# Kernel tuning notes

Hardware: AMD Instinct MI355X
Metric: run time of the kernel (lower is better)

Reference implementation:

```python
import jax, jax.numpy as jnp
import numpy as np

N_NODES = 50000
N_EDGES = 1600000
F_IN = 128
HIDDEN = 128
NUM_GRAPHS = 64


def _glorot(key, shape):
    fan_in = shape[0]
    return (jax.random.normal(key, shape, dtype=jnp.float32) / np.sqrt(fan_in)).astype(jnp.float32)


def setup_inputs() -> dict:
    key = jax.random.key(0)
    ks = jax.random.split(key, 16)
    x = jax.random.normal(ks[0], (N_NODES, F_IN), dtype=jnp.float32)
    edge_index = jax.random.randint(ks[1], (2, N_EDGES), 0, N_NODES, dtype=jnp.int64)
    batch = jnp.sort(jax.random.randint(ks[2], (N_NODES,), 0, NUM_GRAPHS, dtype=jnp.int64))
    # SAGEConv params: lin_l acts on aggregated neighbors, lin_r on root features.
    params = {
        'Wl0': _glorot(ks[3], (F_IN, HIDDEN)), 'Wr0': _glorot(ks[4], (F_IN, HIDDEN)), 'b0': jnp.zeros((HIDDEN,), jnp.float32),
        'Wl1': _glorot(ks[5], (HIDDEN, HIDDEN)), 'Wr1': _glorot(ks[6], (HIDDEN, HIDDEN)), 'b1': jnp.zeros((HIDDEN,), jnp.float32),
        'Wl2': _glorot(ks[7], (HIDDEN, HIDDEN)), 'Wr2': _glorot(ks[8], (HIDDEN, HIDDEN)), 'b2': jnp.zeros((HIDDEN,), jnp.float32),
        'W_lin1': _glorot(ks[9], (3 * HIDDEN, HIDDEN)), 'b_lin1': jnp.zeros((HIDDEN,), jnp.float32),
        'W_lin2': _glorot(ks[10], (HIDDEN, 2)), 'b_lin2': jnp.zeros((2,), jnp.float32),
    }
    return {'x': x, 'edge_index': edge_index, 'batch': batch, **params}


def _sage_conv(x, src, dst, Wl, Wr, b):
    # mean-aggregate neighbor (source) features at target nodes
    n = x.shape[0]
    deg = jax.ops.segment_sum(jnp.ones(src.shape, x.dtype), dst, num_segments=n)
    agg = jax.ops.segment_sum(x[src], dst, num_segments=n)
    agg = agg / jnp.maximum(deg, 1.0)[:, None]
    return agg @ Wl + x @ Wr + b


def reference(x, edge_index, batch,
              Wl0, Wr0, b0, Wl1, Wr1, b1, Wl2, Wr2, b2,
              W_lin1, b_lin1, W_lin2, b_lin2):
    src, dst = edge_index[0], edge_index[1]
    h = jax.nn.relu(_sage_conv(x, src, dst, Wl0, Wr0, b0))
    h = jax.nn.relu(_sage_conv(h, src, dst, Wl1, Wr1, b1))
    h = jax.nn.relu(_sage_conv(h, src, dst, Wl2, Wr2, b2))
    # global add / mean / max pool over graph ids
    add_p = jax.ops.segment_sum(h, batch, num_segments=NUM_GRAPHS)
    cnt = jax.ops.segment_sum(jnp.ones((h.shape[0],), h.dtype), batch, num_segments=NUM_GRAPHS)
    mean_p = add_p / jnp.maximum(cnt, 1.0)[:, None]
    max_p = jax.ops.segment_max(h, batch, num_segments=NUM_GRAPHS)
    g = jnp.concatenate([add_p, mean_p, max_p], axis=1)  # [G, 3*hidden]
    g = jax.nn.relu(g @ W_lin1 + b_lin1)
    # dropout p=0.5 is identity in eval mode
    logits = g @ W_lin2 + b_lin2
    return jax.nn.log_softmax(logits, axis=-1)
```

## Files before the change

kernel.cpp:

```cpp
#include <hip/hip_runtime.h>
#include <hip/hip_bf16.h>

#define N_NODES   50000
#define ZROW      N_NODES
#define F         128
#define NGRAPH    64
#define NB        391
#define B1        400
#define PADMAX    384

typedef __attribute__((ext_vector_type(8))) short    bf16x8;
typedef __attribute__((ext_vector_type(4))) float    f32x4;
typedef __attribute__((ext_vector_type(4))) unsigned u32x4;

__global__ __launch_bounds__(256) void bucket_hist(const int* __restrict__ dst,
                                                   int* __restrict__ bh, int nE, int chunk) {
    __shared__ int hist[NB];
    for (int i = threadIdx.x; i < NB; i += 256) hist[i] = 0;
    __syncthreads();
    int e0 = blockIdx.x * chunk;
    int e1 = min(e0 + chunk, nE);
    for (int e = e0 + threadIdx.x; e < e1; e += 256)
        atomicAdd(&hist[dst[e] >> 7], 1);
    __syncthreads();
    for (int i = threadIdx.x; i < NB; i += 256)
        bh[i * B1 + blockIdx.x] = hist[i];
}

__global__ __launch_bounds__(512) void scan_blocks(const int* __restrict__ bh,
                                                   int* __restrict__ boff,
                                                   int* __restrict__ btot) {
    __shared__ int s[512];
    int bkt = blockIdx.x, t = threadIdx.x;
    int v = (t < B1) ? bh[bkt * B1 + t] : 0;
    s[t] = v;
    __syncthreads();
    for (int off = 1; off < 512; off <<= 1) {
        int u = (t >= off) ? s[t - off] : 0;
        __syncthreads();
        s[t] += u;
        __syncthreads();
    }
    if (t < B1) boff[bkt * B1 + t] = s[t] - v;
    if (t == B1 - 1) btot[bkt] = s[t];
}

__global__ __launch_bounds__(512) void scan_buckets(const int* __restrict__ btot,
                                                    int* __restrict__ bbase) {
    __shared__ int s[512];
    int t = threadIdx.x;
    int v = (t < NB) ? btot[t] : 0;
    s[t] = v;
    __syncthreads();
    for (int off = 1; off < 512; off <<= 1) {
        int u = (t >= off) ? s[t - off] : 0;
        __syncthreads();
        s[t] += u;
        __syncthreads();
    }
    if (t < NB) bbase[t] = s[t] - v;
    if (t == NB - 1) bbase[NB] = s[t];
}

__global__ __launch_bounds__(256) void bucket_place(const int* __restrict__ src,
                                                    const int* __restrict__ dst,
                                                    const int* __restrict__ boff,
                                                    const int* __restrict__ bbase,
                                                    ushort2* __restrict__ ebuf, int nE, int chunk) {
    __shared__ int cur[NB];
    for (int i = threadIdx.x; i < NB; i += 256)
        cur[i] = bbase[i] + boff[i * B1 + blockIdx.x];
    __syncthreads();
    int e0 = blockIdx.x * chunk;
    int e1 = min(e0 + chunk, nE);
    for (int e = e0 + threadIdx.x; e < e1; e += 256) {
        int d = dst[e];
        int pos = atomicAdd(&cur[d >> 7], 1);
        ebuf[pos] = make_ushort2((unsigned short)src[e], (unsigned short)(d & 127));
    }
}

__global__ __launch_bounds__(256) void csr_build(const ushort2* __restrict__ ebuf,
                                                 const int* __restrict__ bbase,
                                                 int* __restrict__ row_ptr,
                                                 int* __restrict__ deg_arr,
                                                 unsigned short* __restrict__ csr, int n) {
    __shared__ int hist[128];
    __shared__ int cursor[128];
    __shared__ int pend[128];
    int b = blockIdx.x, t = threadIdx.x;
    int e0 = bbase[b], e1 = bbase[b + 1];
    if (t < 128) hist[t] = 0;
    __syncthreads();
    for (int e = e0 + t; e < e1; e += 256)
        atomicAdd(&hist[ebuf[e].y], 1);
    __syncthreads();
    if (t == 0) {
        int run = e0 + b * PADMAX;
        #pragma unroll 4
        for (int i = 0; i < 128; ++i) { cursor[i] = run; run += (hist[i] + 3) & ~3; }
    }
    __syncthreads();
    int node = b * 128 + t;
    if (t < 128) {
        pend[t] = cursor[t] + ((hist[t] + 3) & ~3);
        if (node < n) { row_ptr[node] = cursor[t]; deg_arr[node] = hist[t]; }
    }
    __syncthreads();
    for (int e = e0 + t; e < e1; e += 256) {
        ushort2 ed = ebuf[e];
        int pos = atomicAdd(&cursor[ed.y], 1);
        csr[pos] = ed.x;
    }
    __syncthreads();
    if (t < 128)
        for (int p = cursor[t]; p < pend[t]; ++p) csr[p] = (unsigned short)ZROW;
}

struct bh4 { __hip_bfloat16 a, b, c, d; };
__global__ __launch_bounds__(256) void cvt_kernel(const float* __restrict__ in,
                                                  __hip_bfloat16* __restrict__ out, long n4) {
    long i = (long)blockIdx.x * 256 + threadIdx.x;
    if (i >= n4) return;
    float4 v = ((const float4*)in)[i];
    bh4 o;
    o.a = __float2bfloat16(v.x);
    o.b = __float2bfloat16(v.y);
    o.c = __float2bfloat16(v.z);
    o.d = __float2bfloat16(v.w);
    ((bh4*)out)[i] = o;
}

__global__ __launch_bounds__(64) void zero_rows(__hip_bfloat16* __restrict__ xb,
                                                __hip_bfloat16* __restrict__ h1,
                                                __hip_bfloat16* __restrict__ h2) {
    int t = threadIdx.x;
    if (t < 48) {
        __hip_bfloat16* base = (t < 16) ? xb : (t < 32) ? h1 : h2;
        ((u32x4*)(base + (long)ZROW * F))[t & 15] = (u32x4){0, 0, 0, 0};
    }
}

__device__ __forceinline__ void acc8(float* a, u32x4 v) {
    a[0] += __uint_as_float(v.x << 16); a[1] += __uint_as_float(v.x & 0xffff0000u);
    a[2] += __uint_as_float(v.y << 16); a[3] += __uint_as_float(v.y & 0xffff0000u);
    a[4] += __uint_as_float(v.z << 16); a[5] += __uint_as_float(v.z & 0xffff0000u);
    a[6] += __uint_as_float(v.w << 16); a[7] += __uint_as_float(v.w & 0xffff0000u);
}

__global__ __launch_bounds__(256) void gather_kernel(const __hip_bfloat16* __restrict__ xin,
                                                     const int* __restrict__ row_ptr,
                                                     const int* __restrict__ deg_arr,
                                                     const unsigned short* __restrict__ csr,
                                                     __hip_bfloat16* __restrict__ agg, int n) {
    const int node = blockIdx.x * 4 + (threadIdx.x >> 6);
    if (node >= n) return;
    const int lane = threadIdx.x & 63;
    const int q = lane >> 4;
    const int r = lane & 15;

    const int beg = __builtin_nontemporal_load(&row_ptr[node]);
    const int d   = __builtin_nontemporal_load(&deg_arr[node]);
    const int end = beg + ((d + 3) & ~3);

    const u32x4* __restrict__ xr4 = (const u32x4*)xin;

    float a[8] = {}, b[8] = {};
    int i = beg;
    for (; i + 15 < end; i += 16) {
        int s0 = (int)__builtin_nontemporal_load(&csr[i + q]);
        int s1 = (int)__builtin_nontemporal_load(&csr[i + 4 + q]);
        int s2 = (int)__builtin_nontemporal_load(&csr[i + 8 + q]);
        int s3 = (int)__builtin_nontemporal_load(&csr[i + 12 + q]);
        u32x4 v0 = xr4[(unsigned)s0 * 16u + r];
        u32x4 v1 = xr4[(unsigned)s1 * 16u + r];
        u32x4 v2 = xr4[(unsigned)s2 * 16u + r];
        u32x4 v3 = xr4[(unsigned)s3 * 16u + r];
        acc8(a, v0);
        acc8(b, v1);
        acc8(a, v2);
        acc8(b, v3);
    }
    for (; i < end; i += 4) {
        int s0 = (int)__builtin_nontemporal_load(&csr[i + q]);
        u32x4 v0 = xr4[(unsigned)s0 * 16u + r];
        acc8(a, v0);
    }
    #pragma unroll
    for (int j = 0; j < 8; ++j) a[j] += b[j];

    #pragma unroll
    for (int j = 0; j < 8; ++j) {
        a[j] += __shfl_xor(a[j], 16);
        a[j] += __shfl_xor(a[j], 32);
    }

    if (q == 0) {
        float inv = 1.f / fmaxf((float)d, 1.f);
        u32x4 res;
        #pragma unroll
        for (int k = 0; k < 4; ++k) {
            __hip_bfloat16 lo = __float2bfloat16(a[2 * k]     * inv);
            __hip_bfloat16 hi = __float2bfloat16(a[2 * k + 1] * inv);
            res[k] = (unsigned)*(unsigned short*)&lo | ((unsigned)*(unsigned short*)&hi << 16);
        }
        __builtin_nontemporal_store(res, &((u32x4*)agg)[(long)node * 16 + r]);
    }
}

__global__ __launch_bounds__(256) void wfrag_all(const float* __restrict__ Wl0, const float* __restrict__ Wr0,
                                                 const float* __restrict__ Wl1, const float* __restrict__ Wr1,
                                                 const float* __restrict__ Wl2, const float* __restrict__ Wr2,
                                                 __hip_bfloat16* __restrict__ Wf) {
    int layer = blockIdx.x >> 4;
    int t = (blockIdx.x & 15) * 256 + threadIdx.x;
    const float* Wl = (layer == 0) ? Wl0 : (layer == 1) ? Wl1 : Wl2;
    const float* Wr = (layer == 0) ? Wr0 : (layer == 1) ? Wr1 : Wr2;
    int frag = t >> 6, lane = t & 63;
    int kstep = frag >> 3, ntg = frag & 7;
    int q = lane >> 4, r = lane & 15;
    bf16x8 v;
    #pragma unroll
    for (int j = 0; j < 8; ++j) {
        int krow = kstep * 32 + q * 8 + j;
        int col  = ntg * 16 + r;
        float f  = (krow < 128) ? Wl[krow * F + col] : Wr[(krow - 128) * F + col];
        __hip_bfloat16 h = __float2bfloat16(f);
        v[j] = *(short*)&h;
    }
    ((bf16x8*)(Wf + (long)layer * 32768))[t] = v;
}

__global__ __launch_bounds__(256) void sage_gemm(const __hip_bfloat16* __restrict__ aggb,
                                                 const __hip_bfloat16* __restrict__ hinb,
                                                 const __hip_bfloat16* __restrict__ Wf,
                                                 const float* __restrict__ bias,
                                                 __hip_bfloat16* __restrict__ hout,
                                                 const int* __restrict__ batch,
                                                 float* __restrict__ add_p,
                                                 unsigned* __restrict__ max_p,
                                                 float* __restrict__ cnt,
                                                 int n, int do_pool) {
    __shared__ __align__(16) __hip_bfloat16 sOut[64 * 128];
    __shared__ int sBatch[64];

    const int tid  = threadIdx.x;
    const int base = blockIdx.x * 64;
    const int w    = tid >> 6;
    const int lane = tid & 63;
    const int wr   = w >> 1, wc = w & 1;
    const int q    = lane >> 4, r = lane & 15;
    const int m0   = base + wr * 32;

    if (do_pool && tid < 64 && base + tid < n) sBatch[tid] = batch[base + tid];

    int rowA0 = m0 + r;        if (rowA0 >= n) rowA0 = 0;
    int rowA1 = m0 + 16 + r;   if (rowA1 >= n) rowA1 = 0;
    const long a0 = (long)rowA0 * 128 + q * 8;
    const long a1 = (long)rowA1 * 128 + q * 8;

    f32x4 acc[2][4];
    #pragma unroll
    for (int s = 0; s < 2; ++s)
        #pragma unroll
        for (int t = 0; t < 4; ++t) acc[s][t] = (f32x4){0.f, 0.f, 0.f, 0.f};

    const bf16x8* __restrict__ Wv = (const bf16x8*)Wf;
    #pragma unroll
    for (int kstep = 0; kstep < 8; ++kstep) {
        const __hip_bfloat16* basep = (kstep < 4) ? aggb : hinb;
        const int ko = (kstep & 3) * 32;
        bf16x8 af0 = *(const bf16x8*)(basep + a0 + ko);
        bf16x8 af1 = *(const bf16x8*)(basep + a1 + ko);
        #pragma unroll
        for (int t = 0; t < 4; ++t) {
            bf16x8 bf = Wv[(kstep * 8 + wc * 4 + t) * 64 + lane];
            acc[0][t] = __builtin_amdgcn_mfma_f32_16x16x32_bf16(af0, bf, acc[0][t], 0, 0, 0);
            acc[1][t] = __builtin_amdgcn_mfma_f32_16x16x32_bf16(af1, bf, acc[1][t], 0, 0, 0);
        }
    }

    if (!do_pool) {
        #pragma unroll
        for (int t = 0; t < 4; ++t) {
            int col = wc * 64 + t * 16 + r;
            float bv = bias[col];
            #pragma unroll
            for (int s = 0; s < 2; ++s) {
                #pragma unroll
                for (int j = 0; j < 4; ++j) {
                    int rowD = m0 + s * 16 + q * 4 + j;
                    if (rowD < n) {
                        float v = fmaxf(acc[s][t][j] + bv, 0.f);
                        hout[(long)rowD * F + col] = __float2bfloat16(v);
                    }
                }
            }
        }
    } else {
        #pragma unroll
        for (int t = 0; t < 4; ++t) {
            int col = wc * 64 + t * 16 + r;
            float bv = bias[col];
            #pragma unroll
            for (int s = 0; s < 2; ++s) {
                #pragma unroll
                for (int j = 0; j < 4; ++j) {
                    int rowl = wr * 32 + s * 16 + q * 4 + j;
                    float v = fmaxf(acc[s][t][j] + bv, 0.f);
                    sOut[rowl * 128 + col] = __float2bfloat16(v);
                }
            }
        }
        __syncthreads();
        const int colv = tid & 127, rh = tid >> 7;
        float s = 0.f, mx = 0.f, ct = 0.f;
        int g = -1;
        for (int row = rh * 32; row < rh * 32 + 32; ++row) {
            int m = base + row;
            if (m >= n) break;
            int gm = sBatch[row];
            if (gm != g) {
                if (g >= 0) {
                    atomicAdd(&add_p[g * F + colv], s);
                    atomicMax(&max_p[g * F + colv], __float_as_uint(mx));
                    if (colv == 0) atomicAdd(&cnt[g], ct);
                }
                s = 0.f; mx = 0.f; ct = 0.f; g = gm;
            }
            float v = __bfloat162float(sOut[row * 128 + colv]);
            s += v;
            mx = fmaxf(mx, v);
            ct += 1.f;
        }
        if (g >= 0) {
            atomicAdd(&add_p[g * F + colv], s);
            atomicMax(&max_p[g * F + colv], __float_as_uint(mx));
            if (colv == 0) atomicAdd(&cnt[g], ct);
        }
    }
}

__global__ __launch_bounds__(128) void head_kernel(const float* __restrict__ add_p,
                                                   const float* __restrict__ cnt,
                                                   const unsigned* __restrict__ max_p,
                                                   const float* __restrict__ W1,
                                                   const float* __restrict__ b1,
                                                   const float* __restrict__ W2,
                                                   const float* __restrict__ b2,
                                                   float* __restrict__ out) {
    int g = blockIdx.x, n = threadIdx.x;
    __shared__ float gv[384];
    float a    = add_p[g * F + n];
    float invc = 1.f / fmaxf(cnt[g], 1.f);
    gv[n]       = a;
    gv[128 + n] = a * invc;
    gv[256 + n] = __uint_as_float(max_p[g * F + n]);
    __syncthreads();

    float acc = b1[n];
    #pragma unroll 8
    for (int k = 0; k < 384; ++k) acc += gv[k] * W1[k * F + n];
    float r = fmaxf(acc, 0.f);

    float l0 = r * W2[n * 2 + 0];
    float l1 = r * W2[n * 2 + 1];
    #pragma unroll
    for (int off = 32; off > 0; off >>= 1) {
        l0 += __shfl_down(l0, off);
        l1 += __shfl_down(l1, off);
    }
    __shared__ float part[4];
    if ((n & 63) == 0) { part[(n >> 6) * 2] = l0; part[(n >> 6) * 2 + 1] = l1; }
    __syncthreads();
    if (n == 0) {
        float L0 = part[0] + part[2] + b2[0];
        float L1 = part[1] + part[3] + b2[1];
        float m  = fmaxf(L0, L1);
        float lse = m + logf(expf(L0 - m) + expf(L1 - m));
        out[g * 2 + 0] = L0 - lse;
        out[g * 2 + 1] = L1 - lse;
    }
}

extern "C" void kernel_launch(void* const* d_in, const int* in_sizes, int n_in,
                              void* d_out, int out_size, void* d_ws, size_t ws_size,
                              hipStream_t stream) {
    const float* x     = (const float*)d_in[0];
    const int*   ei    = (const int*)d_in[1];
    const int*   batch = (const int*)d_in[2];
    const float* Wl0 = (const float*)d_in[3];
    const float* Wr0 = (const float*)d_in[4];
    const float* b0  = (const float*)d_in[5];
    const float* Wl1 = (const float*)d_in[6];
    const float* Wr1 = (const float*)d_in[7];
    const float* b1  = (const float*)d_in[8];
    const float* Wl2 = (const float*)d_in[9];
    const float* Wr2 = (const float*)d_in[10];
    const float* b2  = (const float*)d_in[11];
    const float* W_lin1 = (const float*)d_in[12];
    const float* b_lin1 = (const float*)d_in[13];
    const float* W_lin2 = (const float*)d_in[14];
    const float* b_lin2 = (const float*)d_in[15];

    const int nE = in_sizes[1] / 2;
    const int* src = ei;
    const int* dst = ei + nE;

    const long TROWS = N_NODES + 16;
    char* p = (char*)d_ws;
    int*   row_ptr = (int*)p;            p += 50048 * 4;
    int*   deg_arr = (int*)p;            p += 50048 * 4;
    unsigned short* csr = (unsigned short*)p;  p += (((long)nE + (long)NB * PADMAX + 63) & ~63L) * 2;
    int*   bh      = (int*)p;            p += ((long)NB * B1 + 16) * 4;
    int*   boff    = (int*)p;            p += ((long)NB * B1 + 16) * 4;
    int*   btot    = (int*)p;            p += 512 * 4;
    int*   bbase   = (int*)p;            p += 512 * 4;
    __hip_bfloat16* xb   = (__hip_bfloat16*)p; p += TROWS * F * 2;
    __hip_bfloat16* aggb = (__hip_bfloat16*)p; p += TROWS * F * 2;
    __hip_bfloat16* h1b  = (__hip_bfloat16*)p; p += TROWS * F * 2;
    __hip_bfloat16* h2b  = (__hip_bfloat16*)p; p += TROWS * F * 2;
    __hip_bfloat16* Wf   = (__hip_bfloat16*)p; p += 3L * 32768 * 2;
    float* add_p   = (float*)p;          p += NGRAPH * F * 4;
    unsigned* max_p = (unsigned*)p;      p += NGRAPH * F * 4;
    float* cnt     = (float*)p;          p += 256;

    ushort2* ebuf = (ushort2*)aggb;

    const int chunk = (nE + B1 - 1) / B1;
    const int gridG = (N_NODES + 63) / 64;
    const int gridW = (N_NODES + 3) / 4;
    const int gridC = (int)(((long)N_NODES * F / 4 + 255) / 256);

    bucket_hist <<<B1, 256, 0, stream>>>(dst, bh, nE, chunk);
    scan_blocks <<<NB, 512, 0, stream>>>(bh, boff, btot);
    scan_buckets<<<1,  512, 0, stream>>>(btot, bbase);
    bucket_place<<<B1, 256, 0, stream>>>(src, dst, boff, bbase, ebuf, nE, chunk);
    csr_build   <<<NB, 256, 0, stream>>>(ebuf, bbase, row_ptr, deg_arr, csr, N_NODES);

    cvt_kernel<<<gridC, 256, 0, stream>>>(x, xb, (long)N_NODES * F / 4);
    zero_rows<<<1, 64, 0, stream>>>(xb, h1b, h2b);
    wfrag_all<<<48, 256, 0, stream>>>(Wl0, Wr0, Wl1, Wr1, Wl2, Wr2, Wf);
    hipMemsetAsync(add_p, 0, (NGRAPH * F * 2 + NGRAPH) * sizeof(float), stream);

    gather_kernel<<<gridW, 256, 0, stream>>>(xb, row_ptr, deg_arr, csr, aggb, N_NODES);
    sage_gemm<<<gridG, 256, 0, stream>>>(aggb, xb, Wf, b0, h1b,
                                         batch, add_p, max_p, cnt, N_NODES, 0);
    gather_kernel<<<gridW, 256, 0, stream>>>(h1b, row_ptr, deg_arr, csr, aggb, N_NODES);
    sage_gemm<<<gridG, 256, 0, stream>>>(aggb, h1b, Wf + 32768, b1, h2b,
                                         batch, add_p, max_p, cnt, N_NODES, 0);
    gather_kernel<<<gridW, 256, 0, stream>>>(h2b, row_ptr, deg_arr, csr, aggb, N_NODES);
    sage_gemm<<<gridG, 256, 0, stream>>>(aggb, h2b, Wf + 65536, b2, (__hip_bfloat16*)nullptr,
                                         batch, add_p, max_p, cnt, N_NODES, 1);

    head_kernel<<<NGRAPH, 128, 0, stream>>>(add_p, cnt, max_p,
                                            W_lin1, b_lin1, W_lin2, b_lin2,
                                            (float*)d_out);
}
```

Measured before the change: 281.9 us.

## Fuse preprocessing kernels into one launch, shrink histogram blocks, pack row pointer and degree

Merges the bucket histogram, fp32-to-bf16 conversion of x, weight fragment packing, pool zeroing and zero-row setup into a single prep_kernel that dispatches on block index. This removes several launches and the memset, and lets these independent jobs run concurrently. The histogram/placement block count drops from 400 to 128, so the scan uses 128-thread blocks. row_ptr and degree are now interleaved into one int2 array so the gather reads both with a single 64-bit load. Fewer histogram blocks mean each one handles a longer chunk, which may slow the histogram and placement stages.

```diff
diff --git a/kernel.cpp b/kernel.cpp
--- a/kernel.cpp
+++ b/kernel.cpp
@@ -6,42 +6,103 @@
 #define F         128
 #define NGRAPH    64
 #define NB        391
-#define B1        400
+#define B1        128
+#define B1ALLOC   400
 #define PADMAX    384
+
+#define CVT_BLOCKS 6250
+#define P_HIST_END 128
+#define P_CVT_END  (P_HIST_END + CVT_BLOCKS)
+#define P_WF_END   (P_CVT_END + 48)
+#define P_ZERO_END (P_WF_END + 65)
+#define P_GRID     (P_ZERO_END + 1)
+#define POOL_FLOATS (NGRAPH * F * 2 + NGRAPH)
 
 typedef __attribute__((ext_vector_type(8))) short    bf16x8;
 typedef __attribute__((ext_vector_type(4))) float    f32x4;
 typedef __attribute__((ext_vector_type(4))) unsigned u32x4;
 
-__global__ __launch_bounds__(256) void bucket_hist(const int* __restrict__ dst,
-                                                   int* __restrict__ bh, int nE, int chunk) {
-    __shared__ int hist[NB];
-    for (int i = threadIdx.x; i < NB; i += 256) hist[i] = 0;
-    __syncthreads();
-    int e0 = blockIdx.x * chunk;
-    int e1 = min(e0 + chunk, nE);
-    for (int e = e0 + threadIdx.x; e < e1; e += 256)
-        atomicAdd(&hist[dst[e] >> 7], 1);
-    __syncthreads();
-    for (int i = threadIdx.x; i < NB; i += 256)
-        bh[i * B1 + blockIdx.x] = hist[i];
-}
-
-__global__ __launch_bounds__(512) void scan_blocks(const int* __restrict__ bh,
+struct bh4 { __hip_bfloat16 a, b, c, d; };
+
+__global__ __launch_bounds__(256) void prep_kernel(const int* __restrict__ dst, int nE, int chunk,
+                                                   int* __restrict__ bh,
+                                                   const float* __restrict__ x,
+                                                   __hip_bfloat16* __restrict__ xb,
+                                                   const float* __restrict__ Wl0, const float* __restrict__ Wr0,
+                                                   const float* __restrict__ Wl1, const float* __restrict__ Wr1,
+                                                   const float* __restrict__ Wl2, const float* __restrict__ Wr2,
+                                                   __hip_bfloat16* __restrict__ Wf,
+                                                   float* __restrict__ poolz,
+                                                   __hip_bfloat16* __restrict__ h1,
+                                                   __hip_bfloat16* __restrict__ h2) {
+    const int b   = blockIdx.x;
+    const int tid = threadIdx.x;
+
+    if (b < P_HIST_END) {
+        __shared__ int hist[NB];
+        for (int i = tid; i < NB; i += 256) hist[i] = 0;
+        __syncthreads();
+        int e0 = b * chunk;
+        int e1 = min(e0 + chunk, nE);
+        for (int e = e0 + tid; e < e1; e += 256)
+            atomicAdd(&hist[dst[e] >> 7], 1);
+        __syncthreads();
+        for (int i = tid; i < NB; i += 256)
+            bh[i * B1 + b] = hist[i];
+    } else if (b < P_CVT_END) {
+        long i = (long)(b - P_HIST_END) * 256 + tid;
+        float4 v = ((const float4*)x)[i];
+        bh4 o;
+        o.a = __float2bfloat16(v.x);
+        o.b = __float2bfloat16(v.y);
+        o.c = __float2bfloat16(v.z);
+        o.d = __float2bfloat16(v.w);
+        ((bh4*)xb)[i] = o;
+    } else if (b < P_WF_END) {
+        int bb = b - P_CVT_END;
+        int layer = bb >> 4;
+        int t = (bb & 15) * 256 + tid;
+        const float* Wl = (layer == 0) ? Wl0 : (layer == 1) ? Wl1 : Wl2;
+        const float* Wr = (layer == 0) ? Wr0 : (layer == 1) ? Wr1 : Wr2;
+        int frag = t >> 6, lane = t & 63;
+        int kstep = frag >> 3, ntg = frag & 7;
+        int q = lane >> 4, r = lane & 15;
+        bf16x8 v;
+        #pragma unroll
+        for (int j = 0; j < 8; ++j) {
+            int krow = kstep * 32 + q * 8 + j;
+            int col  = ntg * 16 + r;
+            float f  = (krow < 128) ? Wl[krow * F + col] : Wr[(krow - 128) * F + col];
+            __hip_bfloat16 h = __float2bfloat16(f);
+            v[j] = *(short*)&h;
+        }
+        ((bf16x8*)(Wf + (long)layer * 32768))[t] = v;
+    } else if (b < P_ZERO_END) {
+        int idx = (b - P_WF_END) * 256 + tid;
+        if (idx < POOL_FLOATS) poolz[idx] = 0.f;
+    } else {
+        if (tid < 48) {
+            __hip_bfloat16* base = (tid < 16) ? xb : (tid < 32) ? h1 : h2;
+            ((u32x4*)(base + (long)ZROW * F))[tid & 15] = (u32x4){0, 0, 0, 0};
+        }
+    }
+}
+
+__global__ __launch_bounds__(128) void scan_blocks(const int* __restrict__ bh,
                                                    int* __restrict__ boff,
                                                    int* __restrict__ btot) {
-    __shared__ int s[512];
+    __shared__ int s[128];
     int bkt = blockIdx.x, t = threadIdx.x;
-    int v = (t < B1) ? bh[bkt * B1 + t] : 0;
+    int v = bh[bkt * B1 + t];
     s[t] = v;
     __syncthreads();
-    for (int off = 1; off < 512; off <<= 1) {
+    for (int off = 1; off < 128; off <<= 1) {
         int u = (t >= off) ? s[t - off] : 0;
         __syncthreads();
         s[t] += u;
         __syncthreads();
     }
-    if (t < B1) boff[bkt * B1 + t] = s[t] - v;
+    boff[bkt * B1 + t] = s[t] - v;
     if (t == B1 - 1) btot[bkt] = s[t];
 }
 
@@ -82,8 +143,7 @@
 
 __global__ __launch_bounds__(256) void csr_build(const ushort2* __restrict__ ebuf,
                                                  const int* __restrict__ bbase,
-                                                 int* __restrict__ row_ptr,
-                                                 int* __restrict__ deg_arr,
+                                                 int* __restrict__ rpd,
                                                  unsigned short* __restrict__ csr, int n) {
     __shared__ int hist[128];
     __shared__ int cursor[128];
@@ -104,7 +164,7 @@
     int node = b * 128 + t;
     if (t < 128) {
         pend[t] = cursor[t] + ((hist[t] + 3) & ~3);
-        if (node < n) { row_ptr[node] = cursor[t]; deg_arr[node] = hist[t]; }
+        if (node < n) ((int2*)rpd)[node] = make_int2(cursor[t], hist[t]);
     }
     __syncthreads();
     for (int e = e0 + t; e < e1; e += 256) {
@@ -115,30 +175,6 @@
     __syncthreads();
     if (t < 128)
         for (int p = cursor[t]; p < pend[t]; ++p) csr[p] = (unsigned short)ZROW;
-}
-
-struct bh4 { __hip_bfloat16 a, b, c, d; };
-__global__ __launch_bounds__(256) void cvt_kernel(const float* __restrict__ in,
-                                                  __hip_bfloat16* __restrict__ out, long n4) {
-    long i = (long)blockIdx.x * 256 + threadIdx.x;
-    if (i >= n4) return;
-    float4 v = ((const float4*)in)[i];
-    bh4 o;
-    o.a = __float2bfloat16(v.x);
-    o.b = __float2bfloat16(v.y);
-    o.c = __float2bfloat16(v.z);
-    o.d = __float2bfloat16(v.w);
-    ((bh4*)out)[i] = o;
-}
-
-__global__ __launch_bounds__(64) void zero_rows(__hip_bfloat16* __restrict__ xb,
-                                                __hip_bfloat16* __restrict__ h1,
-                                                __hip_bfloat16* __restrict__ h2) {
-    int t = threadIdx.x;
-    if (t < 48) {
-        __hip_bfloat16* base = (t < 16) ? xb : (t < 32) ? h1 : h2;
-        ((u32x4*)(base + (long)ZROW * F))[t & 15] = (u32x4){0, 0, 0, 0};
-    }
 }
 
 __device__ __forceinline__ void acc8(float* a, u32x4 v) {
@@ -149,8 +185,7 @@
 }
 
 __global__ __launch_bounds__(256) void gather_kernel(const __hip_bfloat16* __restrict__ xin,
-                                                     const int* __restrict__ row_ptr,
-                                                     const int* __restrict__ deg_arr,
+                                                     const int* __restrict__ rpd,
                                                      const unsigned short* __restrict__ csr,
                                                      __hip_bfloat16* __restrict__ agg, int n) {
     const int node = blockIdx.x * 4 + (threadIdx.x >> 6);
@@ -159,8 +194,9 @@
     const int q = lane >> 4;
     const int r = lane & 15;
 
-    const int beg = __builtin_nontemporal_load(&row_ptr[node]);
-    const int d   = __builtin_nontemporal_load(&deg_arr[node]);
+    const long rd = __builtin_nontemporal_load((const long*)(rpd + 2 * (long)node));
+    const int beg = (int)rd;
+    const int d   = (int)(rd >> 32);
     const int end = beg + ((d + 3) & ~3);
 
     const u32x4* __restrict__ xr4 = (const u32x4*)xin;
@@ -206,29 +242,6 @@
         }
         __builtin_nontemporal_store(res, &((u32x4*)agg)[(long)node * 16 + r]);
     }
-}
-
-__global__ __launch_bounds__(256) void wfrag_all(const float* __restrict__ Wl0, const float* __restrict__ Wr0,
-                                                 const float* __restrict__ Wl1, const float* __restrict__ Wr1,
-                                                 const float* __restrict__ Wl2, const float* __restrict__ Wr2,
-                                                 __hip_bfloat16* __restrict__ Wf) {
-    int layer = blockIdx.x >> 4;
-    int t = (blockIdx.x & 15) * 256 + threadIdx.x;
-    const float* Wl = (layer == 0) ? Wl0 : (layer == 1) ? Wl1 : Wl2;
-    const float* Wr = (layer == 0) ? Wr0 : (layer == 1) ? Wr1 : Wr2;
-    int frag = t >> 6, lane = t & 63;
-    int kstep = frag >> 3, ntg = frag & 7;
-    int q = lane >> 4, r = lane & 15;
-    bf16x8 v;
-    #pragma unroll
-    for (int j = 0; j < 8; ++j) {
-        int krow = kstep * 32 + q * 8 + j;
-        int col  = ntg * 16 + r;
-        float f  = (krow < 128) ? Wl[krow * F + col] : Wr[(krow - 128) * F + col];
-        __hip_bfloat16 h = __float2bfloat16(f);
-        v[j] = *(short*)&h;
-    }
-    ((bf16x8*)(Wf + (long)layer * 32768))[t] = v;
 }
 
 __global__ __launch_bounds__(256) void sage_gemm(const __hip_bfloat16* __restrict__ aggb,
@@ -409,11 +422,10 @@
 
     const long TROWS = N_NODES + 16;
     char* p = (char*)d_ws;
-    int*   row_ptr = (int*)p;            p += 50048 * 4;
-    int*   deg_arr = (int*)p;            p += 50048 * 4;
+    int*   rpd     = (int*)p;            p += 2 * 50048 * 4;
     unsigned short* csr = (unsigned short*)p;  p += (((long)nE + (long)NB * PADMAX + 63) & ~63L) * 2;
-    int*   bh      = (int*)p;            p += ((long)NB * B1 + 16) * 4;
-    int*   boff    = (int*)p;            p += ((long)NB * B1 + 16) * 4;
+    int*   bh      = (int*)p;            p += ((long)NB * B1ALLOC + 16) * 4;
+    int*   boff    = (int*)p;            p += ((long)NB * B1ALLOC + 16) * 4;
     int*   btot    = (int*)p;            p += 512 * 4;
     int*   bbase   = (int*)p;            p += 512 * 4;
     __hip_bfloat16* xb   = (__hip_bfloat16*)p; p += TROWS * F * 2;
@@ -430,26 +442,22 @@
     const int chunk = (nE + B1 - 1) / B1;
     const int gridG = (N_NODES + 63) / 64;
     const int gridW = (N_NODES + 3) / 4;
-    const int gridC = (int)(((long)N_NODES * F / 4 + 255) / 256);
-
-    bucket_hist <<<B1, 256, 0, stream>>>(dst, bh, nE, chunk);
-    scan_blocks <<<NB, 512, 0, stream>>>(bh, boff, btot);
+
+    prep_kernel <<<P_GRID, 256, 0, stream>>>(dst, nE, chunk, bh, x, xb,
+                                             Wl0, Wr0, Wl1, Wr1, Wl2, Wr2, Wf,
+                                             add_p, h1b, h2b);
+    scan_blocks <<<NB, 128, 0, stream>>>(bh, boff, btot);
     scan_buckets<<<1,  512, 0, stream>>>(btot, bbase);
     bucket_place<<<B1, 256, 0, stream>>>(src, dst, boff, bbase, ebuf, nE, chunk);
-    csr_build   <<<NB, 256, 0, stream>>>(ebuf, bbase, row_ptr, deg_arr, csr, N_NODES);
-
-    cvt_kernel<<<gridC, 256, 0, stream>>>(x, xb, (long)N_NODES * F / 4);
-    zero_rows<<<1, 64, 0, stream>>>(xb, h1b, h2b);
-    wfrag_all<<<48, 256, 0, stream>>>(Wl0, Wr0, Wl1, Wr1, Wl2, Wr2, Wf);
-    hipMemsetAsync(add_p, 0, (NGRAPH * F * 2 + NGRAPH) * sizeof(float), stream);
-
-    gather_kernel<<<gridW, 256, 0, stream>>>(xb, row_ptr, deg_arr, csr, aggb, N_NODES);
+    csr_build   <<<NB, 256, 0, stream>>>(ebuf, bbase, rpd, csr, N_NODES);
+
+    gather_kernel<<<gridW, 256, 0, stream>>>(xb, rpd, csr, aggb, N_NODES);
     sage_gemm<<<gridG, 256, 0, stream>>>(aggb, xb, Wf, b0, h1b,
                                          batch, add_p, max_p, cnt, N_NODES, 0);
-    gather_kernel<<<gridW, 256, 0, stream>>>(h1b, row_ptr, deg_arr, csr, aggb, N_NODES);
+    gather_kernel<<<gridW, 256, 0, stream>>>(h1b, rpd, csr, aggb, N_NODES);
     sage_gemm<<<gridG, 256, 0, stream>>>(aggb, h1b, Wf + 32768, b1, h2b,
                                          batch, add_p, max_p, cnt, N_NODES, 0);
-    gather_kernel<<<gridW, 256, 0, stream>>>(h2b, row_ptr, deg_arr, csr, aggb, N_NODES);
+    gather_kernel<<<gridW, 256, 0, stream>>>(h2b, rpd, csr, aggb, N_NODES);
     sage_gemm<<<gridG, 256, 0, stream>>>(aggb, h2b, Wf + 65536, b2, (__hip_bfloat16*)nullptr,
                                          batch, add_p, max_p, cnt, N_NODES, 1);
 
```

Result: slower. 294.6 us (+4.5%).
